# Kernel tuning notes

Hardware: AMD Instinct MI355X
Metric: run time of the kernel (lower is better)

## Reference

```python
import jax, jax.numpy as jnp
import numpy as np

B, L, E, H, NB, WIN = 128, 512, 512, 8, 2, 64
HD = E // H
EPS = 1e-8


def setup_inputs() -> dict:
    key = jax.random.key(0)
    ks = jax.random.split(key, 10)
    s = 0.02
    return {
        "timeline_mask": jax.random.randint(ks[0], (B, L), 0, 10) == 0,
        "seqs": jax.random.normal(ks[1], (B, L, E), jnp.float32),
        "w_in": jax.random.normal(ks[2], (NB, 3 * E, E), jnp.float32) * s,
        "b_in": jnp.zeros((NB, 3 * E), jnp.float32),
        "w_out": jax.random.normal(ks[3], (NB, E, E), jnp.float32) * s,
        "b_out": jnp.zeros((NB, E), jnp.float32),
        "ln1_g": jnp.ones((NB, E), jnp.float32),
        "ln1_b": jnp.zeros((NB, E), jnp.float32),
        "ln2_g": jnp.ones((NB, E), jnp.float32),
        "ln2_b": jnp.zeros((NB, E), jnp.float32),
        "c1_w": jax.random.normal(ks[4], (NB, E, E), jnp.float32) * s,
        "c1_b": jnp.zeros((NB, E), jnp.float32),
        "c2_w": jax.random.normal(ks[5], (NB, E, E), jnp.float32) * s,
        "c2_b": jnp.zeros((NB, E), jnp.float32),
        "lnf_g": jnp.ones((E,), jnp.float32),
        "lnf_b": jnp.zeros((E,), jnp.float32),
    }


def _ln(x, g, b):
    m = x.mean(-1, keepdims=True)
    v = ((x - m) ** 2).mean(-1, keepdims=True)
    return (x - m) * jax.lax.rsqrt(v + EPS) * g + b


def reference(timeline_mask, seqs, w_in, b_in, w_out, b_out,
              ln1_g, ln1_b, ln2_g, ln2_b, c1_w, c1_b, c2_w, c2_b,
              lnf_g, lnf_b):
    i = jnp.arange(L)
    d = i[:, None] - i[None, :]
    allowed = (d >= 0) & (d < WIN)  # [L, L] bool, True = attend

    keep = (~timeline_mask)[..., None].astype(seqs.dtype)  # [B, L, 1]
    x = seqs * keep
    scale = 1.0 / np.sqrt(HD)
    neg = jnp.asarray(jnp.finfo(seqs.dtype).min, seqs.dtype)

    for blk in range(NB):
        q_in = _ln(x, ln1_g[blk], ln1_b[blk])  # torch: query = LN(seqs), key/value = raw seqs
        wq, wk, wv = jnp.split(w_in[blk], 3, axis=0)
        bq, bk, bv = jnp.split(b_in[blk], 3, axis=0)
        q = (q_in @ wq.T + bq).reshape(B, L, H, HD)
        k = (x @ wk.T + bk).reshape(B, L, H, HD)
        v = (x @ wv.T + bv).reshape(B, L, H, HD)
        scores = jnp.einsum("blhd,bmhd->bhlm", q, k) * scale
        scores = jnp.where(allowed, scores, neg)
        attn = jax.nn.softmax(scores, axis=-1)
        o = jnp.einsum("bhlm,bmhd->blhd", attn, v).reshape(B, L, E)
        o = o @ w_out[blk].T + b_out[blk]
        x = q_in + o  # residual onto the layernormed query, as in the original
        x = _ln(x, ln2_g[blk], ln2_b[blk])
        h = jax.nn.relu(x @ c1_w[blk].T + c1_b[blk])  # Conv1d k=1 == pointwise linear
        x = (h @ c2_w[blk].T + c2_b[blk]) + x
        x = x * keep

    return _ln(x, lnf_g, lnf_b)
```

## Files before the change

### kernel.cpp

```cpp
#include <hip/hip_runtime.h>
#include <cstdint>

#define B_   128
#define L_   512
#define E_   512
#define H_   8
#define HD_  64
#define NB_  2
#define WIN_ 64
#define NROW (B_ * L_)

typedef __attribute__((ext_vector_type(8))) __bf16 bf16x8;
typedef __attribute__((ext_vector_type(4))) float f32x4;

static __device__ __forceinline__ unsigned short f2bf(float f) {
  union { float f; unsigned int u; } c; c.f = f;
  unsigned int u = c.u;
  unsigned int r = (u + 0x7fffu + ((u >> 16) & 1u)) >> 16;
  return (unsigned short)r;
}
static __device__ __forceinline__ float bf2f(unsigned short s) {
  union { unsigned int u; float f; } c; c.u = ((unsigned int)s) << 16; return c.f;
}

static __device__ __forceinline__ void gld_lds16(const unsigned short* g, unsigned short* l) {
  __builtin_amdgcn_global_load_lds((const __attribute__((address_space(1))) void*)g,
                                   (__attribute__((address_space(3))) void*)l, 16, 0, 0);
}

__global__ void detect_mask_kernel(const unsigned char* tm, int* flag) {
  __shared__ int f;
  if (threadIdx.x == 0) f = 0;
  __syncthreads();
  int local = 0;
  for (int i = threadIdx.x; i < NROW; i += blockDim.x)
    if ((i & 3) && tm[i]) local = 1;
  if (local) atomicOr(&f, 1);
  __syncthreads();
  if (threadIdx.x == 0) *flag = f;
}

__global__ void expand_keep_kernel(const void* tmv, const int* flag, float* keepF) {
  int i = blockIdx.x * blockDim.x + threadIdx.x;
  if (i >= NROW) return;
  int m;
  if (*flag) m = ((const unsigned char*)tmv)[i] != 0;
  else       m = ((const int*)tmv)[i] != 0;
  keepF[i] = m ? 0.f : 1.f;
}

__global__ void f2bf_kernel(const float* __restrict__ in, unsigned short* __restrict__ out, int n) {
  int i = blockIdx.x * blockDim.x + threadIdx.x;
  if (i < n) out[i] = f2bf(in[i]);
}

__global__ void f2bf_scale_kernel(const float* __restrict__ in, const float* __restrict__ g,
                                  unsigned short* __restrict__ out, int n) {
  int i = blockIdx.x * blockDim.x + threadIdx.x;
  if (i < n) out[i] = f2bf(in[i] * g[i & (E_ - 1)]);
}

__global__ __launch_bounds__(256) void uc_kernel(const float* __restrict__ W, const float* __restrict__ g,
                                                 const float* __restrict__ b, const float* __restrict__ bias,
                                                 float* __restrict__ U, float* __restrict__ C) {
  int wave = threadIdx.x >> 6, lane = threadIdx.x & 63;
  int j = blockIdx.x * 4 + wave;
  const float* wr = W + (size_t)j * E_;
  float su = 0.f, sc = 0.f;
  for (int k = lane; k < E_; k += 64) { float w = wr[k]; su += w * g[k]; sc += w * b[k]; }
  for (int off = 32; off; off >>= 1) { su += __shfl_xor(su, off); sc += __shfl_xor(sc, off); }
  if (lane == 0) { U[j] = su; C[j] = sc + bias[j]; }
}

__global__ void mask_kernel(const float* __restrict__ seqs, const float* __restrict__ keepF,
                            unsigned short* __restrict__ xB) {
  int i = blockIdx.x * blockDim.x + threadIdx.x;
  int idx = i * 4;
  int row = idx >> 9;
  float k = keepF[row];
  float4 v = *(const float4*)(seqs + idx);
  ushort4 b;
  b.x = f2bf(v.x * k); b.y = f2bf(v.y * k); b.z = f2bf(v.z * k); b.w = f2bf(v.w * k);
  *(ushort4*)(xB + idx) = b;
}

__global__ __launch_bounds__(256) void stats_kernel(const unsigned short* __restrict__ X,
                                                    float* __restrict__ st) {
  int wave = threadIdx.x >> 6, lane = threadIdx.x & 63;
  size_t row = (size_t)blockIdx.x * 4 + wave;
  union { uint4 q; unsigned short s[8]; } raw;
  raw.q = *(const uint4*)(X + row * E_ + lane * 8);
  float s = 0.f, s2 = 0.f;
#pragma unroll
  for (int i = 0; i < 8; ++i) { float v = bf2f(raw.s[i]); s += v; s2 += v * v; }
  for (int off = 32; off; off >>= 1) { s += __shfl_xor(s, off); s2 += __shfl_xor(s2, off); }
  if (lane == 0) {
    float mean = s * (1.f / E_);
    float var  = s2 * (1.f / E_) - mean * mean;
    st[row * 2]     = mean;
    st[row * 2 + 1] = rsqrtf(var + 1e-8f);
  }
}

__global__ __launch_bounds__(256) void ln_kernel(const unsigned short* __restrict__ X,
                                                 const float* __restrict__ g,
                                                 const float* __restrict__ bb,
                                                 unsigned short* outB, float* outF) {
  int wave = threadIdx.x >> 6, lane = threadIdx.x & 63;
  size_t row = (size_t)blockIdx.x * 4 + wave;
  const unsigned short* xr = X + row * E_;
  int e0 = lane * 8;
  union { uint4 q; unsigned short s[8]; } raw;
  raw.q = *(const uint4*)(xr + e0);
  float v[8];
#pragma unroll
  for (int i = 0; i < 8; ++i) v[i] = bf2f(raw.s[i]);
  float s = 0.f, s2 = 0.f;
#pragma unroll
  for (int i = 0; i < 8; ++i) { s += v[i]; s2 += v[i] * v[i]; }
  for (int off = 32; off; off >>= 1) { s += __shfl_xor(s, off); s2 += __shfl_xor(s2, off); }
  float mean = s * (1.f / E_);
  float var  = s2 * (1.f / E_) - mean * mean;
  float rs = rsqrtf(var + 1e-8f);
  float4 g0 = *(const float4*)(g + e0),  g1 = *(const float4*)(g + e0 + 4);
  float4 b0 = *(const float4*)(bb + e0), b1 = *(const float4*)(bb + e0 + 4);
  float gg[8] = {g0.x, g0.y, g0.z, g0.w, g1.x, g1.y, g1.z, g1.w};
  float bv[8] = {b0.x, b0.y, b0.z, b0.w, b1.x, b1.y, b1.z, b1.w};
  float y[8];
#pragma unroll
  for (int i = 0; i < 8; ++i) y[i] = (v[i] - mean) * rs * gg[i] + bv[i];
  if (outB) {
    union { uint4 q; unsigned short s[8]; } pk;
#pragma unroll
    for (int i = 0; i < 8; ++i) pk.s[i] = f2bf(y[i]);
    *(uint4*)(outB + row * E_ + e0) = pk.q;
  }
  if (outF) {
    float4 y0 = {y[0], y[1], y[2], y[3]}, y1 = {y[4], y[5], y[6], y[7]};
    *(float4*)(outF + row * E_ + e0) = y0;
    *(float4*)(outF + row * E_ + e0 + 4) = y1;
  }
}

__global__ __launch_bounds__(256, 4) void gemm_kernel(
    const unsigned short* __restrict__ A, const unsigned short* __restrict__ W,
    const float* __restrict__ bias,
    const float* __restrict__ stats, const float* __restrict__ U, const float* __restrict__ C,
    const unsigned short* __restrict__ resX, const float* __restrict__ resStats,
    const float* __restrict__ resG, const float* __restrict__ resB,
    const float* __restrict__ keepF, unsigned short* __restrict__ outB,
    int K, int M, int relu) {
  __shared__ unsigned short sA[2][128 * 32];
  __shared__ unsigned short sW[2][128 * 32];
  int tid = threadIdx.x;
  int wave = tid >> 6, lane = tid & 63;
  int lm = lane & 15, quad = lane >> 4;

  int gx = gridDim.x;
  int nwg = gx * gridDim.y;
  int orig = blockIdx.y * gx + blockIdx.x;
  int chunk = nwg >> 3;
  int wg = (orig & 7) * chunk + (orig >> 3);
  int bx = wg % gx, by = wg / gx;
  size_t row0 = (size_t)by * 128;
  int col0 = bx * 128;
  int wm = (wave >> 1) * 64, wn = (wave & 1) * 64;

  f32x4 acc[4][4];
  f32x4 z = {0.f, 0.f, 0.f, 0.f};
#pragma unroll
  for (int i = 0; i < 4; ++i)
#pragma unroll
    for (int j = 0; j < 4; ++j) acc[i][j] = z;

  int ar0 = tid >> 2, ak0 = ((tid & 3) ^ ((tid >> 3) & 3)) * 8;
  int soff = (wave * 16) * 32;
  const unsigned short* Ar0 = A + (row0 + ar0) * K + ak0;
  const unsigned short* Ar1 = A + (row0 + ar0 + 64) * K + ak0;
  const unsigned short* Wr0 = W + (size_t)(col0 + ar0) * K + ak0;
  const unsigned short* Wr1 = W + (size_t)(col0 + ar0 + 64) * K + ak0;

  auto stage = [&](int p, int k0) {
    gld_lds16(Ar0 + k0, &sA[p][soff]);
    gld_lds16(Ar1 + k0, &sA[p][soff + 64 * 32]);
    gld_lds16(Wr0 + k0, &sW[p][soff]);
    gld_lds16(Wr1 + k0, &sW[p][soff + 64 * 32]);
  };

  int qA = (quad ^ ((lm >> 1) & 3)) * 8;

  int NT = K >> 5;
  stage(0, 0);
  stage(1, 32);
  asm volatile("s_waitcnt vmcnt(4)" ::: "memory");
  __builtin_amdgcn_sched_barrier(0);
  __builtin_amdgcn_s_barrier();

  for (int t = 0; t < NT; ++t) {
    int p = t & 1;
    bf16x8 af[4], bw[4];
#pragma unroll
    for (int mt = 0; mt < 4; ++mt)
      af[mt] = *(const bf16x8*)&sA[p][(wm + mt * 16 + lm) * 32 + qA];
#pragma unroll
    for (int nt = 0; nt < 4; ++nt)
      bw[nt] = *(const bf16x8*)&sW[p][(wn + nt * 16 + lm) * 32 + qA];
    asm volatile("s_waitcnt lgkmcnt(0)" ::: "memory");
    __builtin_amdgcn_sched_barrier(0);
    __builtin_amdgcn_s_barrier();
    if (t + 2 < NT) stage(p, (t + 2) << 5);
#pragma unroll
    for (int mt = 0; mt < 4; ++mt)
#pragma unroll
      for (int nt = 0; nt < 4; ++nt)
        acc[mt][nt] = __builtin_amdgcn_mfma_f32_16x16x32_bf16(af[mt], bw[nt], acc[mt][nt], 0, 0, 0);
    if (t + 1 < NT) {
      if (t + 2 < NT) asm volatile("s_waitcnt vmcnt(4)" ::: "memory");
      else            asm volatile("s_waitcnt vmcnt(0)" ::: "memory");
      __builtin_amdgcn_sched_barrier(0);
      __builtin_amdgcn_s_barrier();
    }
  }

#pragma unroll
  for (int mt = 0; mt < 4; ++mt) {
#pragma unroll
    for (int r = 0; r < 4; ++r) {
      size_t row = row0 + wm + mt * 16 + quad * 4 + r;
      float kf = keepF ? keepF[row] : 1.f;
      float s0 = 1.f, s1 = 0.f;
      if (stats) {
        float2 ms = *(const float2*)(stats + row * 2);
        s0 = ms.y; s1 = -ms.y * ms.x;
      }
      float r0 = 0.f, r1 = 0.f;
      if (resX) {
        float2 ms = *(const float2*)(resStats + row * 2);
        r0 = ms.y; r1 = -ms.y * ms.x;
      }
#pragma unroll
      for (int nt = 0; nt < 4; ++nt) {
        int col = col0 + wn + nt * 16 + lm;
        float v = s0 * acc[mt][nt][r];
        v += U ? (s1 * U[col] + C[col]) : bias[col];
        if (resX) v += (r0 * bf2f(resX[row * (size_t)M + col]) + r1) * resG[col] + resB[col];
        if (relu) v = fmaxf(v, 0.f);
        v *= kf;
        outB[row * (size_t)M + col] = f2bf(v);
      }
    }
  }
}

#define SQS 72
#define SKS 72
#define SVS 68
#define SPS 136
__global__ __launch_bounds__(256) void attn_kernel(const unsigned short* __restrict__ Q,
                                                   const unsigned short* __restrict__ KV,
                                                   unsigned short* O) {
  __shared__ unsigned short smem[64 * SQS + 128 * SKS + 128 * SVS];
  unsigned short* sQ = smem;
  unsigned short* sK = smem + 64 * SQS;
  unsigned short* sV = smem + 64 * SQS + 128 * SKS;
  unsigned short* sP = smem;

  int i0 = blockIdx.x * 64;
  int h = blockIdx.y;
  int b = blockIdx.z;
  int tid = threadIdx.x;
  size_t qbase  = ((size_t)b * L_) * E_ + h * HD_;
  size_t kvbase = ((size_t)b * L_) * (2 * E_) + h * HD_;

  for (int f = tid; f < 512; f += 256) {
    int r = f >> 3, c = f & 7;
    uint4 v = *(const uint4*)&Q[qbase + (size_t)(i0 + r) * E_ + c * 8];
    *(uint4*)&sQ[r * SQS + c * 8] = v;
  }
  for (int f = tid; f < 1024; f += 256) {
    int r = f >> 3, c = f & 7;
    int j = i0 - 64 + r;
    uint4 v = {0, 0, 0, 0};
    if (j >= 0) v = *(const uint4*)&KV[kvbase + (size_t)j * (2 * E_) + c * 8];
    *(uint4*)&sK[r * SKS + c * 8] = v;
  }
  for (int f = tid; f < 2048; f += 256) {
    int r = f >> 4, c = f & 15;
    int j = i0 - 64 + r;
    uint2 v = {0, 0};
    if (j >= 0) v = *(const uint2*)&KV[kvbase + E_ + (size_t)j * (2 * E_) + c * 4];
    *(uint2*)&sV[r * SVS + c * 4] = v;
  }
  __syncthreads();

  int wave = tid >> 6, lane = tid & 63;
  int lm = lane & 15, quad = lane >> 4;
  int wq = wave * 16;

  f32x4 accs[8];
  f32x4 z4 = {0.f, 0.f, 0.f, 0.f};
#pragma unroll
  for (int nt = 0; nt < 8; ++nt) accs[nt] = z4;
  bf16x8 aq0 = *(const bf16x8*)&sQ[(wq + lm) * SQS + quad * 8];
  bf16x8 aq1 = *(const bf16x8*)&sQ[(wq + lm) * SQS + 32 + quad * 8];
#pragma unroll
  for (int nt = 0; nt < 8; ++nt) {
    bf16x8 bk0 = *(const bf16x8*)&sK[(nt * 16 + lm) * SKS + quad * 8];
    bf16x8 bk1 = *(const bf16x8*)&sK[(nt * 16 + lm) * SKS + 32 + quad * 8];
    accs[nt] = __builtin_amdgcn_mfma_f32_16x16x32_bf16(aq0, bk0, accs[nt], 0, 0, 0);
    accs[nt] = __builtin_amdgcn_mfma_f32_16x16x32_bf16(aq1, bk1, accs[nt], 0, 0, 0);
  }
  __syncthreads();

#pragma unroll
  for (int r = 0; r < 4; ++r) {
    int qi = wq + quad * 4 + r;
    float sv[8];
    float mx = -INFINITY;
#pragma unroll
    for (int nt = 0; nt < 8; ++nt) {
      int jn = nt * 16 + lm;
      int d = qi + 64 - jn;
      int j = i0 - 64 + jn;
      float s = (d >= 0 && d < WIN_ && j >= 0) ? accs[nt][r] * 0.125f : -INFINITY;
      sv[nt] = s;
      mx = fmaxf(mx, s);
    }
#pragma unroll
    for (int off = 1; off <= 8; off <<= 1) mx = fmaxf(mx, __shfl_xor(mx, off));
    float sum = 0.f;
#pragma unroll
    for (int nt = 0; nt < 8; ++nt) {
      float e = __expf(sv[nt] - mx);
      sv[nt] = e;
      sum += e;
    }
#pragma unroll
    for (int off = 1; off <= 8; off <<= 1) sum += __shfl_xor(sum, off);
    float inv = 1.f / sum;
#pragma unroll
    for (int nt = 0; nt < 8; ++nt) accs[nt][r] = sv[nt] * inv;
  }

#pragma unroll
  for (int nt = 0; nt < 8; ++nt)
#pragma unroll
    for (int r = 0; r < 4; ++r)
      sP[(wq + quad * 4 + r) * SPS + nt * 16 + lm] = f2bf(accs[nt][r]);
  __syncthreads();

  f32x4 acco[4];
#pragma unroll
  for (int nt = 0; nt < 4; ++nt) acco[nt] = z4;
#pragma unroll
  for (int kt = 0; kt < 4; ++kt) {
    bf16x8 ap = *(const bf16x8*)&sP[(wq + lm) * SPS + kt * 32 + quad * 8];
    int jb = kt * 32 + quad * 8;
#pragma unroll
    for (int nt = 0; nt < 4; ++nt) {
      union { unsigned short u[8]; bf16x8 v; } bv;
#pragma unroll
      for (int jj = 0; jj < 8; ++jj)
        bv.u[jj] = sV[(jb + jj) * SVS + nt * 16 + lm];
      acco[nt] = __builtin_amdgcn_mfma_f32_16x16x32_bf16(ap, bv.v, acco[nt], 0, 0, 0);
    }
  }
#pragma unroll
  for (int nt = 0; nt < 4; ++nt)
#pragma unroll
    for (int r = 0; r < 4; ++r) {
      int qi = wq + quad * 4 + r;
      O[qbase + (size_t)(i0 + qi) * E_ + nt * 16 + lm] = f2bf(acco[nt][r]);
    }
}

extern "C" void kernel_launch(void* const* d_in, const int* in_sizes, int n_in,
                              void* d_out, int out_size, void* d_ws, size_t ws_size,
                              hipStream_t stream) {
  const void*  tm    = d_in[0];
  const float* seqs  = (const float*)d_in[1];
  const float* w_in  = (const float*)d_in[2];
  const float* b_in  = (const float*)d_in[3];
  const float* w_out = (const float*)d_in[4];
  const float* b_out = (const float*)d_in[5];
  const float* ln1_g = (const float*)d_in[6];
  const float* ln1_b = (const float*)d_in[7];
  const float* ln2_g = (const float*)d_in[8];
  const float* ln2_b = (const float*)d_in[9];
  const float* c1_w  = (const float*)d_in[10];
  const float* c1_b  = (const float*)d_in[11];
  const float* c2_w  = (const float*)d_in[12];
  const float* c2_b  = (const float*)d_in[13];
  const float* lnf_g = (const float*)d_in[14];
  const float* lnf_b = (const float*)d_in[15];

  char* ws = (char*)d_ws;
  size_t off = 0;
  auto alloc = [&](size_t bytes) -> char* {
    char* p = ws + off;
    off += (bytes + 255) & ~(size_t)255;
    return p;
  };
  const size_t NE = (size_t)NROW * E_;
  const size_t EE = (size_t)E_ * E_;
  unsigned short* xb     = (unsigned short*)alloc(NE * 2);
  unsigned short* xmid   = (unsigned short*)alloc(NE * 2);
  unsigned short* qb     = (unsigned short*)alloc(NE * 2);
  unsigned short* kvb    = (unsigned short*)alloc(NE * 4);
  unsigned short* w_in_b = (unsigned short*)alloc((size_t)NB_ * 3 * EE * 2);
  unsigned short* w_out_b= (unsigned short*)alloc((size_t)NB_ * EE * 2);
  unsigned short* wc1b   = (unsigned short*)alloc((size_t)NB_ * EE * 2);
  unsigned short* wc2b   = (unsigned short*)alloc((size_t)NB_ * EE * 2);
  float*          keepF  = (float*)alloc((size_t)NROW * 4);
  float*          st1    = (float*)alloc((size_t)NROW * 2 * 4);
  float*          st2    = (float*)alloc((size_t)NROW * 2 * 4);
  float*          ucb    = (float*)alloc((size_t)NB_ * 4 * E_ * 4);
  int*            flag   = (int*)alloc(256);
  if (off > ws_size) return;

  unsigned short* hb = kvb;

  detect_mask_kernel<<<1, 256, 0, stream>>>((const unsigned char*)tm, flag);
  expand_keep_kernel<<<NROW / 256, 256, 0, stream>>>(tm, flag, keepF);

  for (int blk = 0; blk < NB_; ++blk) {
    const float* wi = w_in + (size_t)blk * 3 * EE;
    f2bf_scale_kernel<<<(int)((EE + 255) / 256), 256, 0, stream>>>(
        wi, ln1_g + blk * E_, w_in_b + (size_t)blk * 3 * EE, (int)EE);
    f2bf_kernel<<<(int)((2 * EE + 255) / 256), 256, 0, stream>>>(
        wi + EE, w_in_b + (size_t)blk * 3 * EE + EE, (int)(2 * EE));
    uc_kernel<<<E_ / 4, 256, 0, stream>>>(wi, ln1_g + blk * E_, ln1_b + blk * E_,
                                          b_in + (size_t)blk * 3 * E_,
                                          ucb + (size_t)blk * 4 * E_, ucb + (size_t)blk * 4 * E_ + E_);
    f2bf_scale_kernel<<<(int)((EE + 255) / 256), 256, 0, stream>>>(
        c1_w + (size_t)blk * EE, ln2_g + blk * E_, wc1b + (size_t)blk * EE, (int)EE);
    uc_kernel<<<E_ / 4, 256, 0, stream>>>(c1_w + (size_t)blk * EE, ln2_g + blk * E_, ln2_b + blk * E_,
                                          c1_b + (size_t)blk * E_,
                                          ucb + (size_t)blk * 4 * E_ + 2 * E_, ucb + (size_t)blk * 4 * E_ + 3 * E_);
  }
  int n_sq = NB_ * (int)EE;
  f2bf_kernel<<<(n_sq + 255) / 256, 256, 0, stream>>>(w_out, w_out_b, n_sq);
  f2bf_kernel<<<(n_sq + 255) / 256, 256, 0, stream>>>(c2_w, wc2b, n_sq);

  mask_kernel<<<(int)(NE / 4 / 256), 256, 0, stream>>>(seqs, keepF, xb);

  dim3 ggrid(E_ / 128, NROW / 128);
  dim3 ggridKV(2 * E_ / 128, NROW / 128);
  for (int blk = 0; blk < NB_; ++blk) {
    const unsigned short* wq  = w_in_b + (size_t)blk * 3 * EE;
    const unsigned short* wkv = wq + EE;
    const float* bkv = b_in + (size_t)blk * 3 * E_ + E_;
    float* Uq  = ucb + (size_t)blk * 4 * E_;
    float* Cq  = Uq + E_;
    float* Uc1 = Uq + 2 * E_;
    float* Cc1 = Uq + 3 * E_;

    stats_kernel<<<NROW / 4, 256, 0, stream>>>(xb, st1);
    gemm_kernel<<<ggrid, 256, 0, stream>>>(xb, wq, nullptr, st1, Uq, Cq,
                                           nullptr, nullptr, nullptr, nullptr,
                                           nullptr, qb, E_, E_, 0);
    gemm_kernel<<<ggridKV, 256, 0, stream>>>(xb, wkv, bkv, nullptr, nullptr, nullptr,
                                             nullptr, nullptr, nullptr, nullptr,
                                             nullptr, kvb, E_, 2 * E_, 0);
    attn_kernel<<<dim3(L_ / 64, H_, B_), 256, 0, stream>>>(qb, kvb, qb);
    gemm_kernel<<<ggrid, 256, 0, stream>>>(qb, w_out_b + (size_t)blk * EE, b_out + blk * E_,
                                           nullptr, nullptr, nullptr,
                                           xb, st1, ln1_g + blk * E_, ln1_b + blk * E_,
                                           nullptr, xmid, E_, E_, 0);
    stats_kernel<<<NROW / 4, 256, 0, stream>>>(xmid, st2);
    gemm_kernel<<<ggrid, 256, 0, stream>>>(xmid, wc1b + (size_t)blk * EE, nullptr, st2, Uc1, Cc1,
                                           nullptr, nullptr, nullptr, nullptr,
                                           nullptr, hb, E_, E_, 1);
    gemm_kernel<<<ggrid, 256, 0, stream>>>(hb, wc2b + (size_t)blk * EE, c2_b + blk * E_,
                                           nullptr, nullptr, nullptr,
                                           xmid, st2, ln2_g + blk * E_, ln2_b + blk * E_,
                                           keepF, xb, E_, E_, 0);
  }
  ln_kernel<<<NROW / 4, 256, 0, stream>>>(xb, lnf_g, lnf_b, nullptr, (float*)d_out);
}
```

Measured before the change: 1.735 ms.

## Fuse Q and KV projections into one QKV GEMM, widen GEMM K-step to 64

The separate Q and KV projection GEMMs are merged into one GEMM over a packed QKV buffer. Per-column-block logic applies the LayerNorm-folded stats only to the Q columns. Attention reads Q, K and V from that packed buffer and writes its output in place, and the out-projection reads it with a strided lda. The GEMM main loop now stages 64-wide K tiles with single-buffer-ahead prefetch, raises wave priority around the MFMAs, and lowers the occupancy hint to 2. This cuts launches and rereads of x, but the doubled LDS and shallower prefetch may lower occupancy and expose more memory latency.

```diff
diff --git a/kernel.cpp b/kernel.cpp
--- a/kernel.cpp
+++ b/kernel.cpp
@@ -9,6 +9,7 @@
 #define NB_  2
 #define WIN_ 64
 #define NROW (B_ * L_)
+#define QKVS (3 * E_)
 
 typedef __attribute__((ext_vector_type(8))) __bf16 bf16x8;
 typedef __attribute__((ext_vector_type(4))) float f32x4;
@@ -142,16 +143,19 @@
   }
 }
 
-__global__ __launch_bounds__(256, 4) void gemm_kernel(
+__global__ __launch_bounds__(256, 2) void gemm_kernel(
     const unsigned short* __restrict__ A, const unsigned short* __restrict__ W,
     const float* __restrict__ bias,
     const float* __restrict__ stats, const float* __restrict__ U, const float* __restrict__ C,
+    int statsCols,
     const unsigned short* __restrict__ resX, const float* __restrict__ resStats,
     const float* __restrict__ resG, const float* __restrict__ resB,
     const float* __restrict__ keepF, unsigned short* __restrict__ outB,
-    int K, int M, int relu) {
-  __shared__ unsigned short sA[2][128 * 32];
-  __shared__ unsigned short sW[2][128 * 32];
+    int K, int lda, int M, int relu) {
+  __shared__ unsigned short sA0[2][128 * 32];
+  __shared__ unsigned short sA1[2][128 * 32];
+  __shared__ unsigned short sW0[2][128 * 32];
+  __shared__ unsigned short sW1[2][128 * 32];
   int tid = threadIdx.x;
   int wave = tid >> 6, lane = tid & 63;
   int lm = lane & 15, quad = lane >> 4;
@@ -175,53 +179,63 @@
 
   int ar0 = tid >> 2, ak0 = ((tid & 3) ^ ((tid >> 3) & 3)) * 8;
   int soff = (wave * 16) * 32;
-  const unsigned short* Ar0 = A + (row0 + ar0) * K + ak0;
-  const unsigned short* Ar1 = A + (row0 + ar0 + 64) * K + ak0;
+  const unsigned short* Ar0 = A + (row0 + ar0) * lda + ak0;
+  const unsigned short* Ar1 = A + (row0 + ar0 + 64) * lda + ak0;
   const unsigned short* Wr0 = W + (size_t)(col0 + ar0) * K + ak0;
   const unsigned short* Wr1 = W + (size_t)(col0 + ar0 + 64) * K + ak0;
 
   auto stage = [&](int p, int k0) {
-    gld_lds16(Ar0 + k0, &sA[p][soff]);
-    gld_lds16(Ar1 + k0, &sA[p][soff + 64 * 32]);
-    gld_lds16(Wr0 + k0, &sW[p][soff]);
-    gld_lds16(Wr1 + k0, &sW[p][soff + 64 * 32]);
+    gld_lds16(Ar0 + k0,      &sA0[p][soff]);
+    gld_lds16(Ar1 + k0,      &sA0[p][soff + 64 * 32]);
+    gld_lds16(Ar0 + k0 + 32, &sA1[p][soff]);
+    gld_lds16(Ar1 + k0 + 32, &sA1[p][soff + 64 * 32]);
+    gld_lds16(Wr0 + k0,      &sW0[p][soff]);
+    gld_lds16(Wr1 + k0,      &sW0[p][soff + 64 * 32]);
+    gld_lds16(Wr0 + k0 + 32, &sW1[p][soff]);
+    gld_lds16(Wr1 + k0 + 32, &sW1[p][soff + 64 * 32]);
   };
 
   int qA = (quad ^ ((lm >> 1) & 3)) * 8;
 
-  int NT = K >> 5;
+  int NT = K >> 6;
   stage(0, 0);
-  stage(1, 32);
-  asm volatile("s_waitcnt vmcnt(4)" ::: "memory");
+  asm volatile("s_waitcnt vmcnt(0)" ::: "memory");
   __builtin_amdgcn_sched_barrier(0);
   __builtin_amdgcn_s_barrier();
 
   for (int t = 0; t < NT; ++t) {
     int p = t & 1;
-    bf16x8 af[4], bw[4];
-#pragma unroll
-    for (int mt = 0; mt < 4; ++mt)
-      af[mt] = *(const bf16x8*)&sA[p][(wm + mt * 16 + lm) * 32 + qA];
-#pragma unroll
-    for (int nt = 0; nt < 4; ++nt)
-      bw[nt] = *(const bf16x8*)&sW[p][(wn + nt * 16 + lm) * 32 + qA];
+    if (t + 1 < NT) stage(p ^ 1, (t + 1) << 6);
+    bf16x8 a0[4], a1[4], b0[4], b1[4];
+#pragma unroll
+    for (int mt = 0; mt < 4; ++mt) {
+      a0[mt] = *(const bf16x8*)&sA0[p][(wm + mt * 16 + lm) * 32 + qA];
+      a1[mt] = *(const bf16x8*)&sA1[p][(wm + mt * 16 + lm) * 32 + qA];
+    }
+#pragma unroll
+    for (int nt = 0; nt < 4; ++nt) {
+      b0[nt] = *(const bf16x8*)&sW0[p][(wn + nt * 16 + lm) * 32 + qA];
+      b1[nt] = *(const bf16x8*)&sW1[p][(wn + nt * 16 + lm) * 32 + qA];
+    }
     asm volatile("s_waitcnt lgkmcnt(0)" ::: "memory");
     __builtin_amdgcn_sched_barrier(0);
-    __builtin_amdgcn_s_barrier();
-    if (t + 2 < NT) stage(p, (t + 2) << 5);
+    __builtin_amdgcn_s_setprio(1);
 #pragma unroll
     for (int mt = 0; mt < 4; ++mt)
 #pragma unroll
-      for (int nt = 0; nt < 4; ++nt)
-        acc[mt][nt] = __builtin_amdgcn_mfma_f32_16x16x32_bf16(af[mt], bw[nt], acc[mt][nt], 0, 0, 0);
+      for (int nt = 0; nt < 4; ++nt) {
+        acc[mt][nt] = __builtin_amdgcn_mfma_f32_16x16x32_bf16(a0[mt], b0[nt], acc[mt][nt], 0, 0, 0);
+        acc[mt][nt] = __builtin_amdgcn_mfma_f32_16x16x32_bf16(a1[mt], b1[nt], acc[mt][nt], 0, 0, 0);
+      }
+    __builtin_amdgcn_s_setprio(0);
     if (t + 1 < NT) {
-      if (t + 2 < NT) asm volatile("s_waitcnt vmcnt(4)" ::: "memory");
-      else            asm volatile("s_waitcnt vmcnt(0)" ::: "memory");
+      asm volatile("s_waitcnt vmcnt(0)" ::: "memory");
       __builtin_amdgcn_sched_barrier(0);
       __builtin_amdgcn_s_barrier();
     }
   }
 
+  bool useStats = (stats != nullptr) && (col0 < statsCols);
 #pragma unroll
   for (int mt = 0; mt < 4; ++mt) {
 #pragma unroll
@@ -229,7 +243,7 @@
       size_t row = row0 + wm + mt * 16 + quad * 4 + r;
       float kf = keepF ? keepF[row] : 1.f;
       float s0 = 1.f, s1 = 0.f;
-      if (stats) {
+      if (useStats) {
         float2 ms = *(const float2*)(stats + row * 2);
         s0 = ms.y; s1 = -ms.y * ms.x;
       }
@@ -242,7 +256,7 @@
       for (int nt = 0; nt < 4; ++nt) {
         int col = col0 + wn + nt * 16 + lm;
         float v = s0 * acc[mt][nt][r];
-        v += U ? (s1 * U[col] + C[col]) : bias[col];
+        v += useStats ? (s1 * U[col] + C[col]) : bias[col];
         if (resX) v += (r0 * bf2f(resX[row * (size_t)M + col]) + r1) * resG[col] + resB[col];
         if (relu) v = fmaxf(v, 0.f);
         v *= kf;
@@ -256,9 +270,7 @@
 #define SKS 72
 #define SVS 68
 #define SPS 136
-__global__ __launch_bounds__(256) void attn_kernel(const unsigned short* __restrict__ Q,
-                                                   const unsigned short* __restrict__ KV,
-                                                   unsigned short* O) {
+__global__ __launch_bounds__(256) void attn_kernel(unsigned short* __restrict__ QKV) {
   __shared__ unsigned short smem[64 * SQS + 128 * SKS + 128 * SVS];
   unsigned short* sQ = smem;
   unsigned short* sK = smem + 64 * SQS;
@@ -269,26 +281,25 @@
   int h = blockIdx.y;
   int b = blockIdx.z;
   int tid = threadIdx.x;
-  size_t qbase  = ((size_t)b * L_) * E_ + h * HD_;
-  size_t kvbase = ((size_t)b * L_) * (2 * E_) + h * HD_;
+  size_t base = ((size_t)b * L_) * QKVS + h * HD_;
 
   for (int f = tid; f < 512; f += 256) {
     int r = f >> 3, c = f & 7;
-    uint4 v = *(const uint4*)&Q[qbase + (size_t)(i0 + r) * E_ + c * 8];
+    uint4 v = *(const uint4*)&QKV[base + (size_t)(i0 + r) * QKVS + c * 8];
     *(uint4*)&sQ[r * SQS + c * 8] = v;
   }
   for (int f = tid; f < 1024; f += 256) {
     int r = f >> 3, c = f & 7;
     int j = i0 - 64 + r;
     uint4 v = {0, 0, 0, 0};
-    if (j >= 0) v = *(const uint4*)&KV[kvbase + (size_t)j * (2 * E_) + c * 8];
+    if (j >= 0) v = *(const uint4*)&QKV[base + E_ + (size_t)j * QKVS + c * 8];
     *(uint4*)&sK[r * SKS + c * 8] = v;
   }
   for (int f = tid; f < 2048; f += 256) {
     int r = f >> 4, c = f & 15;
     int j = i0 - 64 + r;
     uint2 v = {0, 0};
-    if (j >= 0) v = *(const uint2*)&KV[kvbase + E_ + (size_t)j * (2 * E_) + c * 4];
+    if (j >= 0) v = *(const uint2*)&QKV[base + 2 * E_ + (size_t)j * QKVS + c * 4];
     *(uint2*)&sV[r * SVS + c * 4] = v;
   }
   __syncthreads();
@@ -370,7 +381,7 @@
 #pragma unroll
     for (int r = 0; r < 4; ++r) {
       int qi = wq + quad * 4 + r;
-      O[qbase + (size_t)(i0 + qi) * E_ + nt * 16 + lm] = f2bf(acco[nt][r]);
+      QKV[base + (size_t)(i0 + qi) * QKVS + nt * 16 + lm] = f2bf(acco[nt][r]);
     }
 }
 
@@ -405,8 +416,7 @@
   const size_t EE = (size_t)E_ * E_;
   unsigned short* xb     = (unsigned short*)alloc(NE * 2);
   unsigned short* xmid   = (unsigned short*)alloc(NE * 2);
-  unsigned short* qb     = (unsigned short*)alloc(NE * 2);
-  unsigned short* kvb    = (unsigned short*)alloc(NE * 4);
+  unsigned short* qkvb   = (unsigned short*)alloc(NE * 6);
   unsigned short* w_in_b = (unsigned short*)alloc((size_t)NB_ * 3 * EE * 2);
   unsigned short* w_out_b= (unsigned short*)alloc((size_t)NB_ * EE * 2);
   unsigned short* wc1b   = (unsigned short*)alloc((size_t)NB_ * EE * 2);
@@ -418,7 +428,7 @@
   int*            flag   = (int*)alloc(256);
   if (off > ws_size) return;
 
-  unsigned short* hb = kvb;
+  unsigned short* hb = qkvb;
 
   detect_mask_kernel<<<1, 256, 0, stream>>>((const unsigned char*)tm, flag);
   expand_keep_kernel<<<NROW / 256, 256, 0, stream>>>(tm, flag, keepF);
@@ -445,36 +455,32 @@
   mask_kernel<<<(int)(NE / 4 / 256), 256, 0, stream>>>(seqs, keepF, xb);
 
   dim3 ggrid(E_ / 128, NROW / 128);
-  dim3 ggridKV(2 * E_ / 128, NROW / 128);
+  dim3 ggridQKV(3 * E_ / 128, NROW / 128);
   for (int blk = 0; blk < NB_; ++blk) {
-    const unsigned short* wq  = w_in_b + (size_t)blk * 3 * EE;
-    const unsigned short* wkv = wq + EE;
-    const float* bkv = b_in + (size_t)blk * 3 * E_ + E_;
+    const unsigned short* wqkv = w_in_b + (size_t)blk * 3 * EE;
+    const float* bqkv = b_in + (size_t)blk * 3 * E_;
     float* Uq  = ucb + (size_t)blk * 4 * E_;
     float* Cq  = Uq + E_;
     float* Uc1 = Uq + 2 * E_;
     float* Cc1 = Uq + 3 * E_;
 
     stats_kernel<<<NROW / 4, 256, 0, stream>>>(xb, st1);
-    gemm_kernel<<<ggrid, 256, 0, stream>>>(xb, wq, nullptr, st1, Uq, Cq,
+    gemm_kernel<<<ggridQKV, 256, 0, stream>>>(xb, wqkv, bqkv, st1, Uq, Cq, E_,
+                                              nullptr, nullptr, nullptr, nullptr,
+                                              nullptr, qkvb, E_, E_, 3 * E_, 0);
+    attn_kernel<<<dim3(L_ / 64, H_, B_), 256, 0, stream>>>(qkvb);
+    gemm_kernel<<<ggrid, 256, 0, stream>>>(qkvb, w_out_b + (size_t)blk * EE, b_out + blk * E_,
+                                           nullptr, nullptr, nullptr, 0,
+                                           xb, st1, ln1_g + blk * E_, ln1_b + blk * E_,
+                                           nullptr, xmid, E_, 3 * E_, E_, 0);
+    stats_kernel<<<NROW / 4, 256, 0, stream>>>(xmid, st2);
+    gemm_kernel<<<ggrid, 256, 0, stream>>>(xmid, wc1b + (size_t)blk * EE, nullptr, st2, Uc1, Cc1, E_,
                                            nullptr, nullptr, nullptr, nullptr,
-                                           nullptr, qb, E_, E_, 0);
-    gemm_kernel<<<ggridKV, 256, 0, stream>>>(xb, wkv, bkv, nullptr, nullptr, nullptr,
-                                             nullptr, nullptr, nullptr, nullptr,
-                                             nullptr, kvb, E_, 2 * E_, 0);
-    attn_kernel<<<dim3(L_ / 64, H_, B_), 256, 0, stream>>>(qb, kvb, qb);
-    gemm_kernel<<<ggrid, 256, 0, stream>>>(qb, w_out_b + (size_t)blk * EE, b_out + blk * E_,
-                                           nullptr, nullptr, nullptr,
-                                           xb, st1, ln1_g + blk * E_, ln1_b + blk * E_,
-                                           nullptr, xmid, E_, E_, 0);
-    stats_kernel<<<NROW / 4, 256, 0, stream>>>(xmid, st2);
-    gemm_kernel<<<ggrid, 256, 0, stream>>>(xmid, wc1b + (size_t)blk * EE, nullptr, st2, Uc1, Cc1,
-                                           nullptr, nullptr, nullptr, nullptr,
-                                           nullptr, hb, E_, E_, 1);
+                                           nullptr, hb, E_, E_, E_, 1);
     gemm_kernel<<<ggrid, 256, 0, stream>>>(hb, wc2b + (size_t)blk * EE, c2_b + blk * E_,
-                                           nullptr, nullptr, nullptr,
+                                           nullptr, nullptr, nullptr, 0,
                                            xmid, st2, ln2_g + blk * E_, ln2_b + blk * E_,
-                                           keepF, xb, E_, E_, 0);
+                                           keepF, xb, E_, E_, E_, 0);
   }
   ln_kernel<<<NROW / 4, 256, 0, stream>>>(xb, lnf_g, lnf_b, nullptr, (float*)d_out);
 }
```

After: 2.189 ms. +26.2%, slower.
